# Performance work log

Hardware: AMD Instinct MI355X
Metric: run time of the kernel (lower is better)

## Reference

```python
import jax, jax.numpy as jnp
import numpy as np

B, T, V, C, NB, NOPS = 8, 2048, 4096, 128, 64, 8

_NONLIN = [
    lambda h: h,
    jax.nn.relu,
    lambda h: jax.nn.gelu(h, approximate=False),
    lambda h: jnp.square(h),
    lambda h: -h,
    jnp.abs,
    jnp.tanh,
    jax.nn.sigmoid,
]


def setup_inputs() -> dict:
    key = jax.random.key(0)
    ks = jax.random.split(key, 6)
    s = 0.02
    return {
        "x": jax.random.normal(ks[0], (B, T, V), dtype=jnp.float32),
        "basis": jax.random.normal(ks[1], (V, 2 * NB), dtype=jnp.float32),
        "read_coeffs": jax.random.normal(ks[2], (C, 2 * NB), dtype=jnp.float32) * s,
        "write_coeffs": jax.random.normal(ks[3], (C, 2 * NB), dtype=jnp.float32) * s,
        "op_logits": jnp.zeros((NOPS,), dtype=jnp.float32),
        "op_weights": jax.random.normal(ks[4], (NOPS, C, C), dtype=jnp.float32) * s,
        "op_biases": jnp.zeros((NOPS, C), dtype=jnp.float32),
        "out_scale": jnp.float32(0.1),
    }


def op_bank(values, op_logits, op_weights, op_biases):
    # values: (B, T, C); soft mixture of 8 small channel transforms
    w = jax.nn.softmax(op_logits)  # (n_ops,)
    result = jnp.zeros_like(values)
    for i in range(NOPS):
        h = values @ op_weights[i] + op_biases[i]
        h = _NONLIN[i % len(_NONLIN)](h)
        result = result + w[i] * h
    return result


def reference(x, basis, read_coeffs, write_coeffs, op_logits, op_weights, op_biases, out_scale):
    # READ: Fourier soft addressing over V registers, normalized over registers (axis 0)
    read_w = jax.nn.softmax(basis @ read_coeffs.T, axis=0)  # (V, C)
    values = x @ read_w  # (B, T, C)
    # SELECT OP + APPLY
    values = op_bank(values, op_logits, op_weights, op_biases)
    # WRITE: unnormalized Fourier addressing back to registers
    write_w = basis @ write_coeffs.T  # (V, C)
    return (values @ write_w.T) * out_scale  # (B, T, V)
```

## Files before the change

### kernel.cpp

```cpp
#include <hip/hip_runtime.h>
#include <math.h>

#define M_TOT 16384
#define V_DIM 4096
#define C_DIM 128

typedef __bf16 bf16;
typedef __bf16 bf16x8 __attribute__((ext_vector_type(8)));
typedef float f32x4 __attribute__((ext_vector_type(4)));

__device__ inline f32x4 zero4() { f32x4 z; z[0]=0.f; z[1]=0.f; z[2]=0.f; z[3]=0.f; return z; }

__device__ inline bf16 f2bf(float f) {
  union { float f; unsigned u; } a; a.f = f;
  unsigned r = (a.u + 0x7FFFu + ((a.u >> 16) & 1u)) >> 16;
  union { unsigned short s; bf16 b; } o; o.s = (unsigned short)r;
  return o.b;
}

__device__ inline bf16x8 cvt8(float4 a, float4 b) {
  bf16x8 r;
  r[0]=f2bf(a.x); r[1]=f2bf(a.y); r[2]=f2bf(a.z); r[3]=f2bf(a.w);
  r[4]=f2bf(b.x); r[5]=f2bf(b.y); r[6]=f2bf(b.z); r[7]=f2bf(b.w);
  return r;
}

__device__ inline void gld_lds16(const void* g, void* l) {
  __builtin_amdgcn_global_load_lds((const __attribute__((address_space(1))) void*)g,
                                   (__attribute__((address_space(3))) void*)l, 16, 0, 0);
}

union PrepU {
  struct { bf16 A[128][136]; bf16 B[128][136]; } lg;
  struct { bf16 A[64][136];  bf16 B[128][136]; } w2;
};

__global__ __launch_bounds__(256) void k_prep(const float* __restrict__ basis,
                                              const float* __restrict__ rc,
                                              const float* __restrict__ wc,
                                              const float* __restrict__ opw,
                                              float* __restrict__ LT,
                                              bf16* __restrict__ W2,
                                              bf16* __restrict__ WTO) {
  __shared__ __align__(16) PrepU pu;
  const int t = threadIdx.x;
  const int bid = blockIdx.x;
  const int lane = t & 63, wave = t >> 6, fm = lane & 15, quad = lane >> 4;

  if (bid < 32) {
    const int v0 = bid * 128;
    {
      const int row = t >> 1, c0 = (t & 1) * 64;
      const float4* p = (const float4*)(rc + row * 128 + c0);
      bf16x8* d = (bf16x8*)&pu.lg.A[row][c0];
#pragma unroll
      for (int j = 0; j < 8; j++) { float4 a = p[2*j], b = p[2*j+1]; d[j] = cvt8(a, b); }
    }
    {
      const int row = t >> 1, c0 = (t & 1) * 64;
      const float4* p = (const float4*)(basis + (size_t)(v0 + row) * 128 + c0);
      bf16x8* d = (bf16x8*)&pu.lg.B[row][c0];
#pragma unroll
      for (int j = 0; j < 8; j++) { float4 a = p[2*j], b = p[2*j+1]; d[j] = cvt8(a, b); }
    }
    __syncthreads();

    f32x4 acc[2][8];
#pragma unroll
    for (int m = 0; m < 2; m++)
#pragma unroll
      for (int n = 0; n < 8; n++) acc[m][n] = zero4();

#pragma unroll
    for (int kk = 0; kk < 4; kk++) {
      bf16x8 af[2];
#pragma unroll
      for (int m = 0; m < 2; m++)
        af[m] = *(const bf16x8*)&pu.lg.A[wave * 32 + m * 16 + fm][kk * 32 + quad * 8];
#pragma unroll
      for (int nt = 0; nt < 8; nt++) {
        bf16x8 bfr = *(const bf16x8*)&pu.lg.B[nt * 16 + fm][kk * 32 + quad * 8];
#pragma unroll
        for (int m = 0; m < 2; m++)
          acc[m][nt] = __builtin_amdgcn_mfma_f32_16x16x32_bf16(af[m], bfr, acc[m][nt], 0, 0, 0);
      }
    }
#pragma unroll
    for (int m = 0; m < 2; m++)
#pragma unroll
      for (int nt = 0; nt < 8; nt++)
#pragma unroll
        for (int r = 0; r < 4; r++) {
          int c = wave * 32 + m * 16 + quad * 4 + r;
          LT[(size_t)c * V_DIM + v0 + nt * 16 + fm] = acc[m][nt][r];
        }
  } else if (bid < 96) {
    const int v0 = (bid - 32) * 64;
    {
      const int row = t >> 2, c0 = (t & 3) * 32;
      const float4* p = (const float4*)(basis + (size_t)(v0 + row) * 128 + c0);
      bf16x8* d = (bf16x8*)&pu.w2.A[row][c0];
#pragma unroll
      for (int j = 0; j < 4; j++) { float4 a = p[2*j], b = p[2*j+1]; d[j] = cvt8(a, b); }
    }
    {
      const int row = t >> 1, c0 = (t & 1) * 64;
      const float4* p = (const float4*)(wc + row * 128 + c0);
      bf16x8* d = (bf16x8*)&pu.w2.B[row][c0];
#pragma unroll
      for (int j = 0; j < 8; j++) { float4 a = p[2*j], b = p[2*j+1]; d[j] = cvt8(a, b); }
    }
    __syncthreads();

    f32x4 acc[8];
#pragma unroll
    for (int n = 0; n < 8; n++) acc[n] = zero4();
#pragma unroll
    for (int kk = 0; kk < 4; kk++) {
      bf16x8 af = *(const bf16x8*)&pu.w2.A[wave * 16 + fm][kk * 32 + quad * 8];
#pragma unroll
      for (int nt = 0; nt < 8; nt++) {
        bf16x8 bfr = *(const bf16x8*)&pu.w2.B[nt * 16 + fm][kk * 32 + quad * 8];
        acc[nt] = __builtin_amdgcn_mfma_f32_16x16x32_bf16(af, bfr, acc[nt], 0, 0, 0);
      }
    }
#pragma unroll
    for (int nt = 0; nt < 8; nt++)
#pragma unroll
      for (int r = 0; r < 4; r++) {
        int v = v0 + wave * 16 + quad * 4 + r;
        W2[v * 128 + nt * 16 + fm] = f2bf(acc[nt][r]);
      }
  } else {
    int idx = (bid - 96) * 256 + t;
    int i = idx >> 14, rem = idx & 16383, n = rem >> 7, k = rem & 127;
    WTO[idx] = f2bf(opw[(i << 14) + k * 128 + n]);
  }
}

__global__ __launch_bounds__(256) void k_softmax(const float* __restrict__ LT,
                                                 bf16* __restrict__ RT) {
  const int c = blockIdx.x, t = threadIdx.x;
  __shared__ float red[256];
  const float* row = LT + (size_t)c * V_DIM;
  float e[16];
  float lmax = -3.0e38f;
#pragma unroll
  for (int j = 0; j < 16; j++) { e[j] = row[t + 256 * j]; lmax = fmaxf(lmax, e[j]); }
  red[t] = lmax;
  __syncthreads();
  for (int off = 128; off > 0; off >>= 1) {
    if (t < off) red[t] = fmaxf(red[t], red[t + off]);
    __syncthreads();
  }
  const float gmax = red[0];
  __syncthreads();
  float lsum = 0.f;
#pragma unroll
  for (int j = 0; j < 16; j++) { e[j] = __expf(e[j] - gmax); lsum += e[j]; }
  red[t] = lsum;
  __syncthreads();
  for (int off = 128; off > 0; off >>= 1) {
    if (t < off) red[t] += red[t + off];
    __syncthreads();
  }
  const float inv = 1.f / red[0];
#pragma unroll
  for (int j = 0; j < 16; j++)
    RT[(size_t)c * V_DIM + t + 256 * j] = f2bf(e[j] * inv);
}

__device__ inline float apply_nonlin(int i, float v) {
  switch (i) {
    case 0: return v;
    case 1: return fmaxf(v, 0.f);
    case 2: return 0.5f * v * (1.f + erff(v * 0.70710678118654752f));
    case 3: return v * v;
    case 4: return -v;
    case 5: return fabsf(v);
    case 6: return tanhf(v);
    default: return 1.f / (1.f + __expf(-v));
  }
}

union MainU {
  bf16 B2[2][128][64];
  bf16 Bp[2][128][136];
};

__global__ __launch_bounds__(256, 1) void k_main(const float* __restrict__ x,
                                                 const bf16* __restrict__ RT,
                                                 const bf16* __restrict__ WTO,
                                                 const bf16* __restrict__ W2,
                                                 const float* __restrict__ op_logits,
                                                 const float* __restrict__ op_biases,
                                                 const float* __restrict__ p_scale,
                                                 float* __restrict__ out) {
  __shared__ __align__(16) MainU mu;
  __shared__ __align__(16) bf16 S[64][136];
  const int t = threadIdx.x;
  const int m0 = blockIdx.x * 64;
  const int lane = t & 63, wave = t >> 6;
  const int fm = lane & 15, quad = lane >> 4;
  const int sw = (fm & 7) << 4;

  const int c_row = wave * 32 + (lane >> 3);
  const int src_colbyte = ((lane & 7) * 16) ^ ((lane >> 3) << 4);
  const bf16* bp = RT + (size_t)c_row * V_DIM + (src_colbyte >> 1);
  const float* xp = x + (size_t)(m0 + wave * 16 + fm) * V_DIM + quad * 8;

  f32x4 acc[8];
#pragma unroll
  for (int i = 0; i < 8; i++) acc[i] = zero4();

#define G1_ISSUE_B(buf, koff)                                                  \
  {                                                                            \
    _Pragma("unroll")                                                          \
    for (int jj = 0; jj < 4; jj++)                                             \
      gld_lds16(bp + (size_t)jj * 8 * V_DIM + (koff),                          \
                (char*)&mu.B2[buf][0][0] + (wave * 4 + jj) * 1024);            \
  }

#define G1_ISSUE_A(p0, p1, p2, p3, koff)                                       \
  {                                                                            \
    p0 = *(const float4*)(xp + (koff));                                        \
    p1 = *(const float4*)(xp + (koff) + 4);                                    \
    p2 = *(const float4*)(xp + (koff) + 32);                                   \
    p3 = *(const float4*)(xp + (koff) + 36);                                   \
  }

#define G1_COMPUTE(buf, p0, p1, p2, p3)                                        \
  {                                                                            \
    bf16x8 af0 = cvt8(p0, p1);                                                 \
    bf16x8 af1 = cvt8(p2, p3);                                                 \
    const char* bb = (const char*)&mu.B2[buf][0][0];                           \
    _Pragma("unroll")                                                          \
    for (int nt = 0; nt < 8; nt++) {                                           \
      const char* rp = bb + (nt * 16 + fm) * 128;                              \
      bf16x8 b0 = *(const bf16x8*)(rp + ((quad * 16) ^ sw));                   \
      bf16x8 b1 = *(const bf16x8*)(rp + ((64 + quad * 16) ^ sw));              \
      acc[nt] = __builtin_amdgcn_mfma_f32_16x16x32_bf16(af0, b0, acc[nt], 0, 0, 0); \
      acc[nt] = __builtin_amdgcn_mfma_f32_16x16x32_bf16(af1, b1, acc[nt], 0, 0, 0); \
    }                                                                          \
  }

  float4 aE0, aE1, aE2, aE3, aO0, aO1, aO2, aO3;

  G1_ISSUE_B(0, 0);
  G1_ISSUE_A(aE0, aE1, aE2, aE3, 0);

  for (int s = 0; s < 32; s++) {
    const int k0 = s * 128;
    __syncthreads();
    G1_ISSUE_B(1, k0 + 64);
    G1_ISSUE_A(aO0, aO1, aO2, aO3, k0 + 64);
    G1_COMPUTE(0, aE0, aE1, aE2, aE3);
    __syncthreads();
    if (s < 31) {
      G1_ISSUE_B(0, k0 + 128);
      G1_ISSUE_A(aE0, aE1, aE2, aE3, k0 + 128);
    }
    G1_COMPUTE(1, aO0, aO1, aO2, aO3);
  }
#undef G1_ISSUE_B
#undef G1_ISSUE_A
#undef G1_COMPUTE

#pragma unroll
  for (int nt = 0; nt < 8; nt++)
#pragma unroll
    for (int r = 0; r < 4; r++)
      S[wave * 16 + quad * 4 + r][nt * 16 + fm] = f2bf(acc[nt][r]);

  float w[8];
  {
    float lm = -3.0e38f;
#pragma unroll
    for (int i = 0; i < 8; i++) { w[i] = op_logits[i]; lm = fmaxf(lm, w[i]); }
    float ssum = 0.f;
#pragma unroll
    for (int i = 0; i < 8; i++) { w[i] = __expf(w[i] - lm); ssum += w[i]; }
    float inv = 1.f / ssum;
#pragma unroll
    for (int i = 0; i < 8; i++) w[i] *= inv;
  }

  const int brow = t >> 1, boff = (t & 1) * 64;
  uint4 pv[8];
  {
    const uint4* p = (const uint4*)(WTO + brow * 128 + boff);
#pragma unroll
    for (int j = 0; j < 8; j++) pv[j] = p[j];
  }

  __syncthreads();

  bf16x8 af[4];
#pragma unroll
  for (int kk = 0; kk < 4; kk++)
    af[kk] = *(const bf16x8*)&S[wave * 16 + fm][kk * 32 + quad * 8];

  f32x4 res[8];
#pragma unroll
  for (int nt = 0; nt < 8; nt++) res[nt] = zero4();

#pragma unroll
  for (int i = 0; i < 8; i++) {
    {
      uint4* d = (uint4*)&mu.Bp[i & 1][brow][boff];
#pragma unroll
      for (int j = 0; j < 8; j++) d[j] = pv[j];
    }
    if (i < 7) {
      const uint4* p = (const uint4*)(WTO + (i + 1) * 16384 + brow * 128 + boff);
#pragma unroll
      for (int j = 0; j < 8; j++) pv[j] = p[j];
    }
    __syncthreads();
#pragma unroll
    for (int nt = 0; nt < 8; nt++) {
      f32x4 h = zero4();
#pragma unroll
      for (int kk = 0; kk < 4; kk++) {
        bf16x8 bfr = *(const bf16x8*)&mu.Bp[i & 1][nt * 16 + fm][kk * 32 + quad * 8];
        h = __builtin_amdgcn_mfma_f32_16x16x32_bf16(af[kk], bfr, h, 0, 0, 0);
      }
      float bias = op_biases[i * 128 + nt * 16 + fm];
#pragma unroll
      for (int r = 0; r < 4; r++)
        res[nt][r] += w[i] * apply_nonlin(i, h[r] + bias);
    }
    __syncthreads();
  }

#pragma unroll
  for (int nt = 0; nt < 8; nt++)
#pragma unroll
    for (int r = 0; r < 4; r++)
      S[wave * 16 + quad * 4 + r][nt * 16 + fm] = f2bf(res[nt][r]);

  {
    const uint4* p = (const uint4*)(W2 + brow * 128 + boff);
#pragma unroll
    for (int j = 0; j < 8; j++) pv[j] = p[j];
  }

  __syncthreads();

  bf16x8 af2[4];
#pragma unroll
  for (int kk = 0; kk < 4; kk++)
    af2[kk] = *(const bf16x8*)&S[wave * 16 + fm][kk * 32 + quad * 8];

  const float scale = *p_scale;

#pragma unroll 2
  for (int ti = 0; ti < 32; ti++) {
    {
      uint4* d = (uint4*)&mu.Bp[ti & 1][brow][boff];
#pragma unroll
      for (int j = 0; j < 8; j++) d[j] = pv[j];
    }
    if (ti < 31) {
      const uint4* p = (const uint4*)(W2 + ((size_t)(ti + 1) * 128 + brow) * 128 + boff);
#pragma unroll
      for (int j = 0; j < 8; j++) pv[j] = p[j];
    }
    __syncthreads();
#pragma unroll
    for (int nt = 0; nt < 8; nt++) {
      f32x4 a2 = zero4();
#pragma unroll
      for (int kk = 0; kk < 4; kk++) {
        bf16x8 bfr = *(const bf16x8*)&mu.Bp[ti & 1][nt * 16 + fm][kk * 32 + quad * 8];
        a2 = __builtin_amdgcn_mfma_f32_16x16x32_bf16(af2[kk], bfr, a2, 0, 0, 0);
      }
#pragma unroll
      for (int r = 0; r < 4; r++)
        out[(size_t)(m0 + wave * 16 + quad * 4 + r) * V_DIM + ti * 128 + nt * 16 + fm] =
            a2[r] * scale;
    }
    __syncthreads();
  }
}

extern "C" void kernel_launch(void* const* d_in, const int* in_sizes, int n_in,
                              void* d_out, int out_size, void* d_ws, size_t ws_size,
                              hipStream_t stream) {
  const float* x      = (const float*)d_in[0];
  const float* basis  = (const float*)d_in[1];
  const float* rc     = (const float*)d_in[2];
  const float* wc     = (const float*)d_in[3];
  const float* oplog  = (const float*)d_in[4];
  const float* opw    = (const float*)d_in[5];
  const float* opb    = (const float*)d_in[6];
  const float* oscale = (const float*)d_in[7];
  float* out = (float*)d_out;
  char* ws = (char*)d_ws;

  float* LT  = (float*)(ws);
  bf16* RT   = (bf16*)(ws + 2097152);
  bf16* W2   = (bf16*)(ws + 3145728);
  bf16* WTO  = (bf16*)(ws + 4194304);

  k_prep   <<<608, 256, 0, stream>>>(basis, rc, wc, opw, LT, W2, WTO);
  k_softmax<<<C_DIM, 256, 0, stream>>>(LT, RT);
  k_main   <<<M_TOT / 64, 256, 0, stream>>>(x, RT, WTO, W2, oplog, opb, oscale, out);
}
```

Before: 644.7 us.

## Split K across 8 waves and load weights directly from global, dropping LDS staging

k_main now runs 512 threads. The first GEMM's K dimension is split between two wave halves, whose partial sums are reduced through an fp32 LDS buffer. RT, WTO and W2 fragments are read straight from global memory (relying on L2/cache) instead of being staged through double-buffered LDS with barriers, and the op-bank and output GEMMs split their N dimension across the wave halves. This removes most __syncthreads and LDS copy traffic and raises occupancy, but it adds redundant global/L2 reads of the weights and heavy register use for 16-fragment prefetch buffers.

```diff
diff --git a/kernel.cpp b/kernel.cpp
--- a/kernel.cpp
+++ b/kernel.cpp
@@ -23,11 +23,6 @@
   r[0]=f2bf(a.x); r[1]=f2bf(a.y); r[2]=f2bf(a.z); r[3]=f2bf(a.w);
   r[4]=f2bf(b.x); r[5]=f2bf(b.y); r[6]=f2bf(b.z); r[7]=f2bf(b.w);
   return r;
-}
-
-__device__ inline void gld_lds16(const void* g, void* l) {
-  __builtin_amdgcn_global_load_lds((const __attribute__((address_space(1))) void*)g,
-                                   (__attribute__((address_space(3))) void*)l, 16, 0, 0);
 }
 
 union PrepU {
@@ -183,12 +178,7 @@
   }
 }
 
-union MainU {
-  bf16 B2[2][128][64];
-  bf16 Bp[2][128][136];
-};
-
-__global__ __launch_bounds__(256, 1) void k_main(const float* __restrict__ x,
+__global__ __launch_bounds__(512, 2) void k_main(const float* __restrict__ x,
                                                  const bf16* __restrict__ RT,
                                                  const bf16* __restrict__ WTO,
                                                  const bf16* __restrict__ W2,
@@ -196,81 +186,80 @@
                                                  const float* __restrict__ op_biases,
                                                  const float* __restrict__ p_scale,
                                                  float* __restrict__ out) {
-  __shared__ __align__(16) MainU mu;
+  __shared__ float R[64][132];
   __shared__ __align__(16) bf16 S[64][136];
   const int t = threadIdx.x;
   const int m0 = blockIdx.x * 64;
   const int lane = t & 63, wave = t >> 6;
   const int fm = lane & 15, quad = lane >> 4;
-  const int sw = (fm & 7) << 4;
-
-  const int c_row = wave * 32 + (lane >> 3);
-  const int src_colbyte = ((lane & 7) * 16) ^ ((lane >> 3) << 4);
-  const bf16* bp = RT + (size_t)c_row * V_DIM + (src_colbyte >> 1);
-  const float* xp = x + (size_t)(m0 + wave * 16 + fm) * V_DIM + quad * 8;
+  const int wg = wave & 3;
+  const int wh = wave >> 2;
+
+  const float* xp = x + (size_t)(m0 + wg * 16 + fm) * V_DIM + wh * 2048 + quad * 8;
+  const bf16*  rp = RT + (size_t)fm * V_DIM + wh * 2048 + quad * 8;
 
   f32x4 acc[8];
 #pragma unroll
   for (int i = 0; i < 8; i++) acc[i] = zero4();
 
-#define G1_ISSUE_B(buf, koff)                                                  \
+#define P1_LA(A0, A1, A2, A3, koff)                                            \
+  {                                                                            \
+    A0 = *(const float4*)(xp + (koff));                                        \
+    A1 = *(const float4*)(xp + (koff) + 4);                                    \
+    A2 = *(const float4*)(xp + (koff) + 32);                                   \
+    A3 = *(const float4*)(xp + (koff) + 36);                                   \
+  }
+#define P1_LB(BB, koff)                                                        \
   {                                                                            \
     _Pragma("unroll")                                                          \
-    for (int jj = 0; jj < 4; jj++)                                             \
-      gld_lds16(bp + (size_t)jj * 8 * V_DIM + (koff),                          \
-                (char*)&mu.B2[buf][0][0] + (wave * 4 + jj) * 1024);            \
-  }
-
-#define G1_ISSUE_A(p0, p1, p2, p3, koff)                                       \
+    for (int nt = 0; nt < 8; nt++) {                                           \
+      BB[2 * nt]     = *(const bf16x8*)(rp + (size_t)nt * 16 * V_DIM + (koff));        \
+      BB[2 * nt + 1] = *(const bf16x8*)(rp + (size_t)nt * 16 * V_DIM + (koff) + 32);   \
+    }                                                                          \
+  }
+#define P1_MM(af0, af1, BB)                                                    \
   {                                                                            \
-    p0 = *(const float4*)(xp + (koff));                                        \
-    p1 = *(const float4*)(xp + (koff) + 4);                                    \
-    p2 = *(const float4*)(xp + (koff) + 32);                                   \
-    p3 = *(const float4*)(xp + (koff) + 36);                                   \
-  }
-
-#define G1_COMPUTE(buf, p0, p1, p2, p3)                                        \
-  {                                                                            \
-    bf16x8 af0 = cvt8(p0, p1);                                                 \
-    bf16x8 af1 = cvt8(p2, p3);                                                 \
-    const char* bb = (const char*)&mu.B2[buf][0][0];                           \
     _Pragma("unroll")                                                          \
     for (int nt = 0; nt < 8; nt++) {                                           \
-      const char* rp = bb + (nt * 16 + fm) * 128;                              \
-      bf16x8 b0 = *(const bf16x8*)(rp + ((quad * 16) ^ sw));                   \
-      bf16x8 b1 = *(const bf16x8*)(rp + ((64 + quad * 16) ^ sw));              \
-      acc[nt] = __builtin_amdgcn_mfma_f32_16x16x32_bf16(af0, b0, acc[nt], 0, 0, 0); \
-      acc[nt] = __builtin_amdgcn_mfma_f32_16x16x32_bf16(af1, b1, acc[nt], 0, 0, 0); \
+      acc[nt] = __builtin_amdgcn_mfma_f32_16x16x32_bf16(af0, BB[2 * nt], acc[nt], 0, 0, 0);     \
+      acc[nt] = __builtin_amdgcn_mfma_f32_16x16x32_bf16(af1, BB[2 * nt + 1], acc[nt], 0, 0, 0); \
     }                                                                          \
   }
 
-  float4 aE0, aE1, aE2, aE3, aO0, aO1, aO2, aO3;
-
-  G1_ISSUE_B(0, 0);
-  G1_ISSUE_A(aE0, aE1, aE2, aE3, 0);
-
-  for (int s = 0; s < 32; s++) {
-    const int k0 = s * 128;
-    __syncthreads();
-    G1_ISSUE_B(1, k0 + 64);
-    G1_ISSUE_A(aO0, aO1, aO2, aO3, k0 + 64);
-    G1_COMPUTE(0, aE0, aE1, aE2, aE3);
-    __syncthreads();
-    if (s < 31) {
-      G1_ISSUE_B(0, k0 + 128);
-      G1_ISSUE_A(aE0, aE1, aE2, aE3, k0 + 128);
-    }
-    G1_COMPUTE(1, aO0, aO1, aO2, aO3);
-  }
-#undef G1_ISSUE_B
-#undef G1_ISSUE_A
-#undef G1_COMPUTE
-
-#pragma unroll
-  for (int nt = 0; nt < 8; nt++)
-#pragma unroll
-    for (int r = 0; r < 4; r++)
-      S[wave * 16 + quad * 4 + r][nt * 16 + fm] = f2bf(acc[nt][r]);
+  {
+    float4 aE0, aE1, aE2, aE3, aO0, aO1, aO2, aO3;
+    bf16x8 BbE[16], BbO[16];
+    P1_LA(aE0, aE1, aE2, aE3, 0);
+    P1_LB(BbE, 0);
+    P1_LA(aO0, aO1, aO2, aO3, 64);
+    P1_LB(BbO, 64);
+    for (int s = 0; s < 16; s++) {
+      const int k0 = s * 128;
+      {
+        bf16x8 af0 = cvt8(aE0, aE1), af1 = cvt8(aE2, aE3);
+        if (s < 15) P1_LA(aE0, aE1, aE2, aE3, k0 + 128);
+        P1_MM(af0, af1, BbE);
+        if (s < 15) P1_LB(BbE, k0 + 128);
+      }
+      {
+        bf16x8 af0 = cvt8(aO0, aO1), af1 = cvt8(aO2, aO3);
+        if (s < 15) P1_LA(aO0, aO1, aO2, aO3, k0 + 192);
+        P1_MM(af0, af1, BbO);
+        if (s < 15) P1_LB(BbO, k0 + 192);
+      }
+    }
+  }
+#undef P1_LA
+#undef P1_LB
+#undef P1_MM
+
+  if (wh == 1) {
+#pragma unroll
+    for (int nt = 0; nt < 8; nt++)
+#pragma unroll
+      for (int r = 0; r < 4; r++)
+        R[wg * 16 + quad * 4 + r][nt * 16 + fm] = acc[nt][r];
+  }
 
   float w[8];
   {
@@ -285,102 +274,77 @@
     for (int i = 0; i < 8; i++) w[i] *= inv;
   }
 
-  const int brow = t >> 1, boff = (t & 1) * 64;
-  uint4 pv[8];
-  {
-    const uint4* p = (const uint4*)(WTO + brow * 128 + boff);
-#pragma unroll
-    for (int j = 0; j < 8; j++) pv[j] = p[j];
-  }
-
+  __syncthreads();
+  if (wh == 0) {
+#pragma unroll
+    for (int nt = 0; nt < 8; nt++)
+#pragma unroll
+      for (int r = 0; r < 4; r++) {
+        float sum = acc[nt][r] + R[wg * 16 + quad * 4 + r][nt * 16 + fm];
+        S[wg * 16 + quad * 4 + r][nt * 16 + fm] = f2bf(sum);
+      }
+  }
   __syncthreads();
 
   bf16x8 af[4];
 #pragma unroll
   for (int kk = 0; kk < 4; kk++)
-    af[kk] = *(const bf16x8*)&S[wave * 16 + fm][kk * 32 + quad * 8];
-
-  f32x4 res[8];
-#pragma unroll
-  for (int nt = 0; nt < 8; nt++) res[nt] = zero4();
+    af[kk] = *(const bf16x8*)&S[wg * 16 + fm][kk * 32 + quad * 8];
+
+  f32x4 res[4];
+#pragma unroll
+  for (int j = 0; j < 4; j++) res[j] = zero4();
 
 #pragma unroll
   for (int i = 0; i < 8; i++) {
-    {
-      uint4* d = (uint4*)&mu.Bp[i & 1][brow][boff];
-#pragma unroll
-      for (int j = 0; j < 8; j++) d[j] = pv[j];
-    }
-    if (i < 7) {
-      const uint4* p = (const uint4*)(WTO + (i + 1) * 16384 + brow * 128 + boff);
-#pragma unroll
-      for (int j = 0; j < 8; j++) pv[j] = p[j];
-    }
-    __syncthreads();
+#pragma unroll
+    for (int j = 0; j < 4; j++) {
+      const int n = (wh * 4 + j) * 16 + fm;
+      const bf16* wp = WTO + i * 16384 + (size_t)n * 128 + quad * 8;
+      f32x4 h = zero4();
+#pragma unroll
+      for (int kk = 0; kk < 4; kk++) {
+        bf16x8 b = *(const bf16x8*)(wp + kk * 32);
+        h = __builtin_amdgcn_mfma_f32_16x16x32_bf16(af[kk], b, h, 0, 0, 0);
+      }
+      const float bias = op_biases[i * 128 + n];
+#pragma unroll
+      for (int r = 0; r < 4; r++)
+        res[j][r] += w[i] * apply_nonlin(i, h[r] + bias);
+    }
+  }
+
+  __syncthreads();
+#pragma unroll
+  for (int j = 0; j < 4; j++)
+#pragma unroll
+    for (int r = 0; r < 4; r++)
+      S[wg * 16 + quad * 4 + r][wh * 64 + j * 16 + fm] = f2bf(res[j][r]);
+  __syncthreads();
+
+  bf16x8 af2[4];
+#pragma unroll
+  for (int kk = 0; kk < 4; kk++)
+    af2[kk] = *(const bf16x8*)&S[wg * 16 + fm][kk * 32 + quad * 8];
+
+  const float scale = *p_scale;
+  const size_t orow = (size_t)(m0 + wg * 16 + quad * 4);
+
+  for (int tt = 0; tt < 16; tt++) {
+    const int ti = wh * 16 + tt;
 #pragma unroll
     for (int nt = 0; nt < 8; nt++) {
-      f32x4 h = zero4();
+      const bf16* wp = W2 + ((size_t)ti * 128 + nt * 16 + fm) * 128 + quad * 8;
+      f32x4 a2 = zero4();
 #pragma unroll
       for (int kk = 0; kk < 4; kk++) {
-        bf16x8 bfr = *(const bf16x8*)&mu.Bp[i & 1][nt * 16 + fm][kk * 32 + quad * 8];
-        h = __builtin_amdgcn_mfma_f32_16x16x32_bf16(af[kk], bfr, h, 0, 0, 0);
-      }
-      float bias = op_biases[i * 128 + nt * 16 + fm];
+        bf16x8 b = *(const bf16x8*)(wp + kk * 32);
+        a2 = __builtin_amdgcn_mfma_f32_16x16x32_bf16(af2[kk], b, a2, 0, 0, 0);
+      }
 #pragma unroll
       for (int r = 0; r < 4; r++)
-        res[nt][r] += w[i] * apply_nonlin(i, h[r] + bias);
-    }
-    __syncthreads();
-  }
-
-#pragma unroll
-  for (int nt = 0; nt < 8; nt++)
-#pragma unroll
-    for (int r = 0; r < 4; r++)
-      S[wave * 16 + quad * 4 + r][nt * 16 + fm] = f2bf(res[nt][r]);
-
-  {
-    const uint4* p = (const uint4*)(W2 + brow * 128 + boff);
-#pragma unroll
-    for (int j = 0; j < 8; j++) pv[j] = p[j];
-  }
-
-  __syncthreads();
-
-  bf16x8 af2[4];
-#pragma unroll
-  for (int kk = 0; kk < 4; kk++)
-    af2[kk] = *(const bf16x8*)&S[wave * 16 + fm][kk * 32 + quad * 8];
-
-  const float scale = *p_scale;
-
-#pragma unroll 2
-  for (int ti = 0; ti < 32; ti++) {
-    {
-      uint4* d = (uint4*)&mu.Bp[ti & 1][brow][boff];
-#pragma unroll
-      for (int j = 0; j < 8; j++) d[j] = pv[j];
-    }
-    if (ti < 31) {
-      const uint4* p = (const uint4*)(W2 + ((size_t)(ti + 1) * 128 + brow) * 128 + boff);
-#pragma unroll
-      for (int j = 0; j < 8; j++) pv[j] = p[j];
-    }
-    __syncthreads();
-#pragma unroll
-    for (int nt = 0; nt < 8; nt++) {
-      f32x4 a2 = zero4();
-#pragma unroll
-      for (int kk = 0; kk < 4; kk++) {
-        bf16x8 bfr = *(const bf16x8*)&mu.Bp[ti & 1][nt * 16 + fm][kk * 32 + quad * 8];
-        a2 = __builtin_amdgcn_mfma_f32_16x16x32_bf16(af2[kk], bfr, a2, 0, 0, 0);
-      }
-#pragma unroll
-      for (int r = 0; r < 4; r++)
-        out[(size_t)(m0 + wave * 16 + quad * 4 + r) * V_DIM + ti * 128 + nt * 16 + fm] =
-            a2[r] * scale;
-    }
-    __syncthreads();
+        out[(orow + r) * V_DIM + ti * 128 + nt * 16 + fm] = a2[r] * scale;
+    }
   }
 }
 
@@ -405,5 +369,5 @@
 
   k_prep   <<<608, 256, 0, stream>>>(basis, rc, wc, opw, LT, W2, WTO);
   k_softmax<<<C_DIM, 256, 0, stream>>>(LT, RT);
-  k_main   <<<M_TOT / 64, 256, 0, stream>>>(x, RT, WTO, W2, oplog, opb, oscale, out);
-}
+  k_main   <<<M_TOT / 64, 512, 0, stream>>>(x, RT, WTO, W2, oplog, opb, oscale, out);
+}
```

Measured after the change: 689.3 us. 6.9% more time.
